# Optimization experiments

Hardware: AMD Instinct MI355X
Metric: run time of the kernel (lower is better)

## Reference

```python
import jax, jax.numpy as jnp
import numpy as np

B, H, W = 2, 192, 192
DIM, HEADS, WS = 192, 6, 16
NT, RD, GS = 128, 20, 128
MLP_HID, TD_F, KS = 384, 48, 5
EPS = 1e-5


def _layernorm(x, g, b):
    m = jnp.mean(x, -1, keepdims=True)
    v = jnp.var(x, -1, keepdims=True)
    return (x - m) / jnp.sqrt(v + EPS) * g + b


def _l2n(x):
    return x / jnp.maximum(jnp.linalg.norm(x, axis=-1, keepdims=True), 1e-12)


def _rpi(ws):
    coords = np.stack(np.meshgrid(np.arange(ws), np.arange(ws), indexing='ij'))
    cf = coords.reshape(2, -1)
    rc = (cf[:, :, None] - cf[:, None, :]).transpose(1, 2, 0)
    rc[..., 0] += ws - 1
    rc[..., 1] += ws - 1
    rc[..., 0] *= 2 * ws - 1
    return rc.sum(-1)  # (ws*ws, ws*ws)


RPI = _rpi(WS)


def _win_attn(qkv, rpb, proj_w, h, w):
    # plain W-MSA (shift_size = 0 -> no mask, no roll)
    b, n, c3 = qkv.shape
    c = c3 // 3
    hd = c // HEADS
    nw = WS * WS
    xw = qkv.reshape(b, h // WS, WS, w // WS, WS, c3).transpose(0, 1, 3, 2, 4, 5).reshape(-1, nw, c3)
    bw = xw.shape[0]
    q, k, v = xw.reshape(bw, nw, 3, HEADS, hd).transpose(2, 0, 3, 1, 4)
    attn = (q * hd ** -0.5) @ k.swapaxes(-2, -1)  # (bw, heads, nw, nw)
    bias = rpb[RPI.reshape(-1)].reshape(nw, nw, HEADS).transpose(2, 0, 1)
    attn = jax.nn.softmax(attn + bias[None])
    out = (attn @ v).swapaxes(1, 2).reshape(bw, nw, c) @ proj_w
    out = out.reshape(b, h // WS, w // WS, WS, WS, c).transpose(0, 1, 3, 2, 4, 5).reshape(b, n, c)
    return out


def _atd_ca(x, td, wq, wk, wv, scale_p):
    q = _l2n(x @ wq)   # (b,n,rd)
    k = _l2n(td @ wk)  # (b,m,rd)
    v = td @ wv        # (b,m,c)
    scale = 1.0 + jnp.clip(scale_p, 0.0, 3.0) * np.log(NT)
    attn = jax.nn.softmax((q @ k.swapaxes(-2, -1)) * scale)  # (b,n,m)
    return attn @ v, attn


def _ac_msa(qkv, tk_id, proj_w):
    b, n, c3 = qkv.shape
    c = c3 // 3
    gs = min(n, GS)
    ng = (n + gs - 1) // gs
    pad = ng * gs - n
    idx = jnp.argsort(tk_id, axis=-1)          # sort tokens by category id
    inv = jnp.argsort(idx, axis=-1)            # inverse permutation
    sq = jnp.take_along_axis(qkv, idx[..., None], axis=1)
    if pad > 0:
        sq = jnp.concatenate([sq, sq[:, n - pad:n][:, ::-1]], axis=1)
    q, k, v = sq.reshape(b, ng, gs, 3, HEADS, c // HEADS).transpose(3, 0, 1, 4, 2, 5)
    attn = jax.nn.softmax((q @ k.swapaxes(-2, -1)) * (c // HEADS) ** -0.5)
    out = (attn @ v).transpose(0, 1, 3, 2, 4).reshape(b, ng * gs, c)[:, :n]
    out = jnp.take_along_axis(out, inv[..., None], axis=1)
    return out @ proj_w


def _convffn(x, x_td, w1, dw, w2, h, w):
    y = jnp.concatenate([jax.nn.gelu(x @ w1, approximate=False), x_td], axis=-1)
    b, n, ch = y.shape
    img = y.swapaxes(1, 2).reshape(b, ch, h, w)
    p = (KS - 1) // 2
    conv = jax.lax.conv_general_dilated(img, dw, (1, 1), [(p, p), (p, p)],
                                        dimension_numbers=('NCHW', 'OIHW', 'NCHW'),
                                        feature_group_count=ch)
    conv = jax.nn.gelu(conv, approximate=False).reshape(b, ch, n).swapaxes(1, 2)
    return (y + conv) @ w2


def setup_inputs():
    key = jax.random.key(0)
    ks = jax.random.split(key, 16)
    p = lambda k, s: jax.random.normal(k, s, jnp.float32) * 0.02
    return {
        'x': jax.random.normal(ks[0], (B, H * W, DIM), jnp.float32),
        'td': jax.random.normal(ks[1], (B, NT, DIM), jnp.float32),
        'norm1_g': jnp.ones((DIM,), jnp.float32), 'norm1_b': jnp.zeros((DIM,), jnp.float32),
        'norm2_g': jnp.ones((DIM,), jnp.float32), 'norm2_b': jnp.zeros((DIM,), jnp.float32),
        'wqkv': p(ks[2], (DIM, 3 * DIM)),
        'rpb': p(ks[3], ((2 * WS - 1) ** 2, HEADS)),
        'win_proj': p(ks[4], (DIM, DIM)),
        'atd_wq': p(ks[5], (DIM, RD)),
        'atd_wk': p(ks[6], (DIM, RD)),
        'atd_wv': p(ks[7], (DIM, DIM)),
        'atd_scale': jnp.ones((1,), jnp.float32),
        'aca_proj': p(ks[8], (DIM, DIM)),
        'fc_td_w': p(ks[9], (DIM, TD_F)),
        'ffn_w1': p(ks[10], (DIM, MLP_HID)),
        'ffn_dw': p(ks[11], (MLP_HID + TD_F, 1, KS, KS)),
        'ffn_w2': p(ks[12], (MLP_HID + TD_F, DIM)),
        'h': H, 'w': W,
    }


def reference(x, td, norm1_g, norm1_b, norm2_g, norm2_b, wqkv, rpb, win_proj,
              atd_wq, atd_wk, atd_wv, atd_scale, aca_proj, fc_td_w,
              ffn_w1, ffn_dw, ffn_w2, h, w):
    shortcut = x
    xn = _layernorm(x, norm1_g, norm1_b)
    qkv = xn @ wqkv  # (b, n, 3c)
    x_atd, sim = _atd_ca(xn, td, atd_wq, atd_wk, atd_wv, atd_scale)
    x_aca = _ac_msa(qkv, jnp.argmax(sim, axis=-1), aca_proj)
    x_win = _win_attn(qkv, rpb, win_proj, h, w)
    x = shortcut + x_win + x_atd + x_aca
    x_td = sim @ (td @ fc_td_w)  # (b, n, td_f): dictionary features routed by cross-attn weights
    x = x + _convffn(_layernorm(x, norm2_g, norm2_b), x_td, ffn_w1, ffn_dw, ffn_w2, h, w)
    return x
```

## Files before the change

kernel.cpp:

```cpp
#include <hip/hip_runtime.h>
#include <hip/hip_bf16.h>
#include <math.h>

#define NTOK 36864
#define NTOT 73728
#define CDIM 192
#define C3   576
#define NH   6
#define HD   32
#define RD   20
#define NTD  128
#define GSZ  128
#define NGRP 288
#define MLP  384
#define TDF  48
#define CH   432
#define RAWLD 384

typedef __hip_bfloat16 bf16;
typedef __attribute__((ext_vector_type(8))) short short8;
typedef __attribute__((ext_vector_type(4))) float f32x4;

__device__ __forceinline__ float gelu_f(float x) {
    return 0.5f * x * (1.0f + erff(x * 0.7071067811865475f));
}

__device__ __forceinline__ unsigned short f32_to_bf16u(float f) {
    unsigned int u = __float_as_uint(f);
    u = (u + 0x7FFFu + ((u >> 16) & 1u)) >> 16;
    return (unsigned short)u;
}

__device__ __forceinline__ unsigned pack2bf(float a, float b) {
    return (unsigned)f32_to_bf16u(a) | ((unsigned)f32_to_bf16u(b) << 16);
}

__device__ __forceinline__ float bfbits2f(unsigned short u) {
    return __uint_as_float(((unsigned)u) << 16);
}

__global__ void pack_bt(const float* __restrict__ src, bf16* __restrict__ dst,
                        int K, int N, int ldk, int koff) {
    int i = blockIdx.x * 256 + threadIdx.x;
    if (i >= K * N) return;
    int k = i / N, n = i - k * N;
    dst[(long)n * ldk + koff + k] = __float2bfloat16(src[i]);
}

template<int WF32>
__global__ void ln_kernel(const float* __restrict__ x, const float* __restrict__ g,
                          const float* __restrict__ be, float* __restrict__ outf,
                          bf16* __restrict__ outh) {
    long tok = (long)blockIdx.x * 4 + (threadIdx.x >> 6);
    int lane = threadIdx.x & 63;
    const float* row = x + tok * CDIM;
    float v0 = row[lane], v1 = row[lane + 64], v2 = row[lane + 128];
    float s  = v0 + v1 + v2;
    float ss = v0 * v0 + v1 * v1 + v2 * v2;
    #pragma unroll
    for (int o = 32; o > 0; o >>= 1) {
        s  += __shfl_down(s, o);
        ss += __shfl_down(ss, o);
    }
    s = __shfl(s, 0); ss = __shfl(ss, 0);
    float mean = s * (1.0f / 192.0f);
    float var  = ss * (1.0f / 192.0f) - mean * mean;
    float rstd = rsqrtf(var + 1e-5f);
    float r0 = (v0 - mean) * rstd * g[lane]       + be[lane];
    float r1 = (v1 - mean) * rstd * g[lane + 64]  + be[lane + 64];
    float r2 = (v2 - mean) * rstd * g[lane + 128] + be[lane + 128];
    if (WF32) {
        float* orow = outf + tok * CDIM;
        orow[lane] = r0; orow[lane + 64] = r1; orow[lane + 128] = r2;
    }
    bf16* hrow = outh + tok * CDIM;
    hrow[lane]       = __float2bfloat16(r0);
    hrow[lane + 64]  = __float2bfloat16(r1);
    hrow[lane + 128] = __float2bfloat16(r2);
}

#define LDT 72
template<int ACC, int GELU, int BF16OUT, int CHUNK8, int ADDX, int PL8OUT = 0>
__global__ void __launch_bounds__(256) gemm_bt(
        const bf16* __restrict__ A, const bf16* __restrict__ Bt,
        void* __restrict__ Cv, const float* __restrict__ Xadd,
        int M, int N, int K, int lda, int ldbt, int ldc) {
    __shared__ short As[128 * LDT];
    __shared__ short Bs[64 * LDT];
    int tid  = threadIdx.x;
    int lane = tid & 63;
    int w    = tid >> 6;
    int wr = w >> 1, wc = w & 1;
    int row0 = blockIdx.y * 128, col0 = blockIdx.x * 64;
    int fr = lane & 15, fq = lane >> 4;
    f32x4 acc[4][2];
    #pragma unroll
    for (int m = 0; m < 4; ++m)
        #pragma unroll
        for (int n = 0; n < 2; ++n) acc[m][n] = (f32x4)(0.0f);

    int sa_row = tid >> 3;
    int sa_kc  = (tid & 7) * 8;
    int sb_col = tid & 63;
    int sb_kb  = (tid >> 6) * 16;
    bool cok = (col0 + sb_col) < N;

    for (int k0 = 0; k0 < K; k0 += 64) {
        __syncthreads();
        int kk = k0 + sa_kc;
        #pragma unroll
        for (int p = 0; p < 4; ++p) {
            int r = sa_row + p * 32;
            short8 v = (short8)(0);
            if (kk + 8 <= K) {
                const bf16* src;
                if (CHUNK8)
                    src = A + ((long)(kk >> 3) * NTOT + row0 + r) * 8;
                else
                    src = A + (long)(row0 + r) * lda + kk;
                v = *(const short8*)src;
            } else if (!CHUNK8 && kk < K) {
                #pragma unroll
                for (int i = 0; i < 8; ++i)
                    v[i] = (kk + i < K) ? *(const short*)&A[(long)(row0 + r) * lda + kk + i]
                                        : (short)0;
            }
            *(short8*)&As[r * LDT + sa_kc] = v;
        }
        {
            short8 v0 = (short8)(0), v1 = (short8)(0);
            if (cok) {
                const bf16* src = Bt + (long)(col0 + sb_col) * ldbt + k0 + sb_kb;
                v0 = *(const short8*)src;
                v1 = *(const short8*)(src + 8);
            }
            *(short8*)&Bs[sb_col * LDT + sb_kb]     = v0;
            *(short8*)&Bs[sb_col * LDT + sb_kb + 8] = v1;
        }
        __syncthreads();
        short8 af[4][2], bf_[2][2];
        #pragma unroll
        for (int m = 0; m < 4; ++m) {
            int r = wr * 64 + m * 16 + fr;
            af[m][0] = *(const short8*)&As[r * LDT + fq * 8];
            af[m][1] = *(const short8*)&As[r * LDT + 32 + fq * 8];
        }
        #pragma unroll
        for (int n = 0; n < 2; ++n) {
            int c = wc * 32 + n * 16 + fr;
            bf_[n][0] = *(const short8*)&Bs[c * LDT + fq * 8];
            bf_[n][1] = *(const short8*)&Bs[c * LDT + 32 + fq * 8];
        }
        #pragma unroll
        for (int m = 0; m < 4; ++m)
            #pragma unroll
            for (int n = 0; n < 2; ++n) {
                acc[m][n] = __builtin_amdgcn_mfma_f32_16x16x32_bf16(
                                af[m][0], bf_[n][0], acc[m][n], 0, 0, 0);
                acc[m][n] = __builtin_amdgcn_mfma_f32_16x16x32_bf16(
                                af[m][1], bf_[n][1], acc[m][n], 0, 0, 0);
            }
    }
    #pragma unroll
    for (int m = 0; m < 4; ++m) {
        #pragma unroll
        for (int n = 0; n < 2; ++n) {
            int gc = col0 + wc * 32 + n * 16 + fr;
            if (gc >= N) continue;
            #pragma unroll
            for (int r = 0; r < 4; ++r) {
                int gr = row0 + wr * 64 + m * 16 + fq * 4 + r;
                float vv = acc[m][n][r];
                if (GELU) vv = gelu_f(vv);
                if (BF16OUT) {
                    long o;
                    if (PL8OUT) o = ((long)(gc >> 3) * NTOT + gr) * 8 + (gc & 7);
                    else        o = (long)gr * ldc + gc;
                    ((bf16*)Cv)[o] = __float2bfloat16(vv);
                } else {
                    long o = (long)gr * ldc + gc;
                    float* Cc = (float*)Cv;
                    if (ADDX) Cc[o] = Xadd[o] + vv;
                    else if (ACC) Cc[o] += vv;
                    else Cc[o] = vv;
                }
            }
        }
    }
}

template<int ACC, int GELU>
__global__ void __launch_bounds__(256) gemm_kernel(
        const float* __restrict__ A, const float* __restrict__ B,
        float* __restrict__ Cc, int M, int N, int K, int lda, int ldb, int ldc) {
    __shared__ float As[16][68];
    __shared__ float Bs[16][68];
    int tid = threadIdx.x;
    int tr = tid >> 4, tc = tid & 15;
    int row0 = blockIdx.y * 64, col0 = blockIdx.x * 64;
    float acc[4][4] = {};
    int lm = tid >> 4;
    int lk = tid & 15;
    int bk = tid >> 6;
    int bn = tid & 63;
    for (int k0 = 0; k0 < K; k0 += 16) {
        #pragma unroll
        for (int i = 0; i < 4; ++i) {
            int m = lm + i * 16;
            int gr = row0 + m;
            As[lk][m] = (gr < M) ? A[(long)gr * lda + (k0 + lk)] : 0.0f;
        }
        #pragma unroll
        for (int i = 0; i < 4; ++i) {
            int kk = bk + i * 4;
            int gc = col0 + bn;
            Bs[kk][bn] = (gc < N) ? B[(long)(k0 + kk) * ldb + gc] : 0.0f;
        }
        __syncthreads();
        #pragma unroll
        for (int kk = 0; kk < 16; ++kk) {
            float4 av = *(const float4*)&As[kk][tr * 4];
            float4 bv = *(const float4*)&Bs[kk][tc * 4];
            float a[4] = {av.x, av.y, av.z, av.w};
            float b[4] = {bv.x, bv.y, bv.z, bv.w};
            #pragma unroll
            for (int i = 0; i < 4; ++i)
                #pragma unroll
                for (int j = 0; j < 4; ++j)
                    acc[i][j] = fmaf(a[i], b[j], acc[i][j]);
        }
        __syncthreads();
    }
    #pragma unroll
    for (int i = 0; i < 4; ++i) {
        int gr = row0 + tr * 4 + i;
        if (gr >= M) continue;
        #pragma unroll
        for (int j = 0; j < 4; ++j) {
            int gc = col0 + tc * 4 + j;
            if (gc >= N) continue;
            float v = acc[i][j];
            if (GELU) v = gelu_f(v);
            long o = (long)gr * ldc + gc;
            if (ACC) Cc[o] += v; else Cc[o] = v;
        }
    }
}

__global__ void __launch_bounds__(256) qn_kernel(
        const float* __restrict__ xn, const float* __restrict__ awq,
        float* __restrict__ qn) {
    __shared__ float aw[192 * RD];
    __shared__ float xs[256 * 33];
    int tid = threadIdx.x;
    long tok0 = (long)blockIdx.x * 256;
    for (int e = tid; e < 192 * RD; e += 256) aw[e] = awq[e];
    float acc[RD];
    #pragma unroll
    for (int j = 0; j < RD; ++j) acc[j] = 0.0f;
    for (int kc = 0; kc < 192; kc += 32) {
        __syncthreads();
        for (int e = tid; e < 256 * 32; e += 256) {
            int tk = e >> 5, kk = e & 31;
            xs[tk * 33 + kk] = xn[(tok0 + tk) * CDIM + kc + kk];
        }
        __syncthreads();
        #pragma unroll 8
        for (int kk = 0; kk < 32; ++kk) {
            float v = xs[tid * 33 + kk];
            const float* ar = &aw[(kc + kk) * RD];
            #pragma unroll
            for (int j = 0; j < RD; ++j) acc[j] = fmaf(v, ar[j], acc[j]);
        }
    }
    float ss = 0.0f;
    #pragma unroll
    for (int j = 0; j < RD; ++j) ss += acc[j] * acc[j];
    float inv = 1.0f / fmaxf(sqrtf(ss), 1e-12f);
    float* orow = qn + (tok0 + tid) * RD;
    #pragma unroll
    for (int j = 0; j < RD; ++j) orow[j] = acc[j] * inv;
}

__global__ void l2n_kernel(float* __restrict__ d, int nrows) {
    int i = blockIdx.x * blockDim.x + threadIdx.x;
    if (i >= nrows) return;
    float* r = d + (long)i * RD;
    float ss = 0.0f;
    #pragma unroll
    for (int k = 0; k < RD; ++k) ss += r[k] * r[k];
    float inv = 1.0f / fmaxf(sqrtf(ss), 1e-12f);
    #pragma unroll
    for (int k = 0; k < RD; ++k) r[k] *= inv;
}

__global__ void __launch_bounds__(128) sim_kernel(
        const float* __restrict__ qn, const float* __restrict__ kn,
        const float* __restrict__ scale_p, bf16* __restrict__ sim,
        int* __restrict__ tkid) {
    int tok = blockIdx.x;
    int b = tok / NTOK;
    int j = threadIdx.x;
    __shared__ float qv[RD];
    __shared__ float wred[4];
    __shared__ int   wredi[2];
    if (j < RD) qv[j] = qn[(long)tok * RD + j];
    __syncthreads();
    const float* kr = kn + ((long)b * NTD + j) * RD;
    float s = 0.0f;
    #pragma unroll
    for (int r = 0; r < RD; ++r) s = fmaf(qv[r], kr[r], s);
    float scl = 1.0f + fminf(fmaxf(scale_p[0], 0.0f), 3.0f) * logf(128.0f);
    s *= scl;
    float m = s; int mi = j;
    #pragma unroll
    for (int o = 32; o > 0; o >>= 1) {
        float om = __shfl_down(m, o); int oi = __shfl_down(mi, o);
        if (om > m || (om == m && oi < mi)) { m = om; mi = oi; }
    }
    int wv = j >> 6;
    if ((j & 63) == 0) { wred[wv] = m; wredi[wv] = mi; }
    __syncthreads();
    float m0 = wred[0], m1 = wred[1];
    float gm; int gi;
    if (m1 > m0) { gm = m1; gi = wredi[1]; } else { gm = m0; gi = wredi[0]; }
    float p = __expf(s - gm);
    float t = p;
    #pragma unroll
    for (int o = 32; o > 0; o >>= 1) t += __shfl_down(t, o);
    if ((j & 63) == 0) wred[2 + wv] = t;
    __syncthreads();
    float tot = wred[2] + wred[3];
    sim[(long)tok * NTD + j] = __float2bfloat16(p / tot);
    if (j == 0) tkid[tok] = gi;
}

__global__ void hist_kernel(const int* __restrict__ tkid, int* __restrict__ hist) {
    int tile = blockIdx.x;
    int tid = threadIdx.x;
    __shared__ int h[NTD];
    h[tid] = 0;
    __syncthreads();
    atomicAdd(&h[tkid[tile * GSZ + tid]], 1);
    __syncthreads();
    hist[tile * NTD + tid] = h[tid];
}

__global__ void scan_kernel(int* __restrict__ hist) {
    int b = blockIdx.x;
    int c = threadIdx.x;
    __shared__ int tot[NTD];
    __shared__ int base[NTD];
    int run = 0;
    for (int t = 0; t < NGRP; ++t) {
        int id = (b * NGRP + t) * NTD + c;
        int v = hist[id];
        hist[id] = run;
        run += v;
    }
    tot[c] = run;
    __syncthreads();
    if (c == 0) {
        int a = 0;
        for (int i = 0; i < NTD; ++i) { base[i] = a; a += tot[i]; }
    }
    __syncthreads();
    int bc = base[c];
    for (int t = 0; t < NGRP; ++t)
        hist[(b * NGRP + t) * NTD + c] += bc;
}

__global__ void scatter_kernel(const int* __restrict__ tkid, const int* __restrict__ hist,
                               int* __restrict__ idxs) {
    int tile = blockIdx.x;
    int b = tile / NGRP;
    int gl = tile % NGRP;
    int tid = threadIdx.x;
    __shared__ int cats[GSZ];
    int cat = tkid[tile * GSZ + tid];
    cats[tid] = cat;
    __syncthreads();
    int rank = 0;
    for (int j = 0; j < tid; ++j) rank += (cats[j] == cat) ? 1 : 0;
    int pos = hist[tile * NTD + cat] + rank;
    idxs[b * NTOK + pos] = gl * GSZ + tid;
}

#define VLDW 264
#define VLDA 136


__global__ void __launch_bounds__(256) win_mfma(
        const bf16* __restrict__ qkv, const float* __restrict__ rpb,
        bf16* __restrict__ raw) {
    int t2  = blockIdx.x;
    int h   = t2 % NH;
    int wid = t2 / NH;
    int b = wid / 144;
    int wrem = wid % 144;
    int wy = wrem / 12, wx = wrem % 12;
    long base_tok = (long)b * NTOK;

    __shared__ short Kt[256 * 40];
    __shared__ short Vt[32 * VLDW];
    __shared__ float rb[961];

    int tid = threadIdx.x;
    int lane = tid & 63;
    int wv = tid >> 6;
    int fr = lane & 15, fq = lane >> 4;
    const float scl = 0.17677669529663687f;

    for (int i = tid; i < 961; i += 256) rb[i] = rpb[i * NH + h];

    short8 qf[4];
    #pragma unroll
    for (int m = 0; m < 4; ++m) {
        int q = wv * 64 + m * 16 + fr;
        long nq = base_tok + (long)(wy * 16 + (q >> 4)) * 192 + (wx * 16 + (q & 15));
        qf[m] = *(const short8*)(qkv + nq * C3 + h * HD + fq * 8);
    }

    {
        int s_ = tid >> 2, ch = tid & 3;
        #pragma unroll
        for (int t = 0; t < 4; ++t) {
            int p = t * 64 + s_;
            long nk = base_tok + (long)(wy * 16 + (p >> 4)) * 192 + (wx * 16 + (p & 15));
            const bf16* kb = qkv + nk * C3 + CDIM + h * HD + ch * 8;
            *(short8*)&Kt[p * 40 + ch * 8] = *(const short8*)kb;
            short8 vv = *(const short8*)(kb + CDIM);
            #pragma unroll
            for (int i = 0; i < 8; ++i)
                Vt[(ch * 8 + i) * VLDW + p] = vv[i];
        }
    }
    __syncthreads();

    f32x4 acc[4][2];
    float lst[4];
    #pragma unroll
    for (int m = 0; m < 4; ++m) {
        acc[m][0] = (f32x4)(0.0f); acc[m][1] = (f32x4)(0.0f);
        lst[m] = 0.0f;
    }

    for (int t = 0; t < 4; ++t) {
        short8 ak[4], av[2][2];
        #pragma unroll
        for (int c = 0; c < 4; ++c)
            ak[c] = *(const short8*)&Kt[(t * 64 + c * 16 + fr) * 40 + fq * 8];
        #pragma unroll
        for (int n = 0; n < 2; ++n)
            #pragma unroll
            for (int ks = 0; ks < 2; ++ks)
                av[n][ks] = *(const short8*)&Vt[(n * 16 + fr) * VLDW + t * 64 + ks * 32 + fq * 8];

        #pragma unroll
        for (int m = 0; m < 4; ++m) {
            int q = wv * 64 + m * 16 + fr;
            int iy = q >> 4, ix = q & 15;
            int bxb = ix + 15 - 4 * fq;
            float s[4][4];
            #pragma unroll
            for (int c = 0; c < 4; ++c) {
                f32x4 s4 = (f32x4)(0.0f);
                s4 = __builtin_amdgcn_mfma_f32_16x16x32_bf16(ak[c], qf[m], s4, 0, 0, 0);
                const float* rbp = &rb[(iy + 15 - (t * 4 + c)) * 31 + bxb];
                #pragma unroll
                for (int r = 0; r < 4; ++r)
                    s[c][r] = s4[r] * scl + rbp[-r];
            }
            float ps = 0.0f;
            #pragma unroll
            for (int c = 0; c < 4; ++c)
                #pragma unroll
                for (int r = 0; r < 4; ++r) {
                    float p = __expf(s[c][r]);
                    s[c][r] = p;
                    ps += p;
                }
            ps += __shfl_xor(ps, 16);
            ps += __shfl_xor(ps, 32);
            lst[m] += ps;
            unsigned pk[4][2];
            #pragma unroll
            for (int c = 0; c < 4; ++c) {
                pk[c][0] = pack2bf(s[c][0], s[c][1]);
                pk[c][1] = pack2bf(s[c][2], s[c][3]);
            }
            #pragma unroll
            for (int ks = 0; ks < 2; ++ks) {
                unsigned u[4];
                #pragma unroll
                for (int jj = 0; jj < 4; ++jj) {
                    int src = fr + 16 * (2 * (fq & 1) + (jj >> 1));
                    unsigned lo = (unsigned)__shfl((int)pk[2 * ks][jj & 1], src);
                    unsigned hi = (unsigned)__shfl((int)pk[2 * ks + 1][jj & 1], src);
                    u[jj] = (fq & 2) ? hi : lo;
                }
                short8 pb;
                #pragma unroll
                for (int jj = 0; jj < 4; ++jj) {
                    pb[2 * jj]     = (short)(u[jj] & 0xFFFF);
                    pb[2 * jj + 1] = (short)(u[jj] >> 16);
                }
                #pragma unroll
                for (int n = 0; n < 2; ++n)
                    acc[m][n] = __builtin_amdgcn_mfma_f32_16x16x32_bf16(
                                    av[n][ks], pb, acc[m][n], 0, 0, 0);
            }
        }
    }
    #pragma unroll
    for (int m = 0; m < 4; ++m) {
        int q = wv * 64 + m * 16 + fr;
        long nq = base_tok + (long)(wy * 16 + (q >> 4)) * 192 + (wx * 16 + (q & 15));
        float inv = 1.0f / lst[m];
        #pragma unroll
        for (int n = 0; n < 2; ++n) {
            uint2 wv2;
            wv2.x = pack2bf(acc[m][n][0] * inv, acc[m][n][1] * inv);
            wv2.y = pack2bf(acc[m][n][2] * inv, acc[m][n][3] * inv);
            *(uint2*)(raw + nq * RAWLD + h * HD + n * 16 + 4 * fq) = wv2;
        }
    }
}

__global__ void __launch_bounds__(128) aca_mfma(
        const bf16* __restrict__ qkv, const int* __restrict__ idxs,
        bf16* __restrict__ raw) {
    int t2   = blockIdx.x;
    int h    = t2 % NH;
    int grp  = t2 / NH;
    int b = grp / NGRP;
    int g = grp % NGRP;
    long btok = (long)b * NTOK;

    __shared__ short Kt[128 * 40];
    __shared__ short Vt[32 * VLDA];
    __shared__ int   sidx[GSZ];

    int tid = threadIdx.x;
    int lane = tid & 63;
    int half = tid >> 6;
    int fr = lane & 15, fq = lane >> 4;
    const float scl = 0.17677669529663687f;

    sidx[tid] = idxs[btok + g * GSZ + tid];
    __syncthreads();

    short8 qf[4];
    #pragma unroll
    for (int m = 0; m < 4; ++m) {
        long n = btok + sidx[half * 64 + m * 16 + fr];
        qf[m] = *(const short8*)(qkv + n * C3 + h * HD + fq * 8);
    }

    {
        int s_ = tid >> 1, hf = tid & 1;
        int d0 = hf * 16;
        #pragma unroll
        for (int t = 0; t < 2; ++t) {
            int p = t * 64 + s_;
            long n = btok + sidx[p];
            const bf16* kb = qkv + n * C3 + CDIM + h * HD + d0;
            *(short8*)&Kt[p * 40 + d0]     = *(const short8*)kb;
            *(short8*)&Kt[p * 40 + d0 + 8] = *(const short8*)(kb + 8);
            short8 v0 = *(const short8*)(kb + CDIM);
            short8 v1 = *(const short8*)(kb + CDIM + 8);
            #pragma unroll
            for (int i = 0; i < 8; ++i) {
                Vt[(d0 + i) * VLDA + p]     = v0[i];
                Vt[(d0 + 8 + i) * VLDA + p] = v1[i];
            }
        }
    }
    __syncthreads();

    f32x4 acc[4][2];
    float lst[4];
    #pragma unroll
    for (int m = 0; m < 4; ++m) {
        acc[m][0] = (f32x4)(0.0f); acc[m][1] = (f32x4)(0.0f);
        lst[m] = 0.0f;
    }

    for (int t = 0; t < 2; ++t) {
        short8 ak[4], av[2][2];
        #pragma unroll
        for (int c = 0; c < 4; ++c)
            ak[c] = *(const short8*)&Kt[(t * 64 + c * 16 + fr) * 40 + fq * 8];
        #pragma unroll
        for (int n = 0; n < 2; ++n)
            #pragma unroll
            for (int ks = 0; ks < 2; ++ks)
                av[n][ks] = *(const short8*)&Vt[(n * 16 + fr) * VLDA + t * 64 + ks * 32 + fq * 8];

        #pragma unroll
        for (int m = 0; m < 4; ++m) {
            float s[4][4];
            #pragma unroll
            for (int c = 0; c < 4; ++c) {
                f32x4 s4 = (f32x4)(0.0f);
                s4 = __builtin_amdgcn_mfma_f32_16x16x32_bf16(ak[c], qf[m], s4, 0, 0, 0);
                #pragma unroll
                for (int r = 0; r < 4; ++r) s[c][r] = s4[r] * scl;
            }
            float ps = 0.0f;
            #pragma unroll
            for (int c = 0; c < 4; ++c)
                #pragma unroll
                for (int r = 0; r < 4; ++r) {
                    float p = __expf(s[c][r]);
                    s[c][r] = p;
                    ps += p;
                }
            ps += __shfl_xor(ps, 16);
            ps += __shfl_xor(ps, 32);
            lst[m] += ps;
            unsigned pk[4][2];
            #pragma unroll
            for (int c = 0; c < 4; ++c) {
                pk[c][0] = pack2bf(s[c][0], s[c][1]);
                pk[c][1] = pack2bf(s[c][2], s[c][3]);
            }
            #pragma unroll
            for (int ks = 0; ks < 2; ++ks) {
                unsigned u[4];
                #pragma unroll
                for (int jj = 0; jj < 4; ++jj) {
                    int src = fr + 16 * (2 * (fq & 1) + (jj >> 1));
                    unsigned lo = (unsigned)__shfl((int)pk[2 * ks][jj & 1], src);
                    unsigned hi = (unsigned)__shfl((int)pk[2 * ks + 1][jj & 1], src);
                    u[jj] = (fq & 2) ? hi : lo;
                }
                short8 pb;
                #pragma unroll
                for (int jj = 0; jj < 4; ++jj) {
                    pb[2 * jj]     = (short)(u[jj] & 0xFFFF);
                    pb[2 * jj + 1] = (short)(u[jj] >> 16);
                }
                #pragma unroll
                for (int n = 0; n < 2; ++n)
                    acc[m][n] = __builtin_amdgcn_mfma_f32_16x16x32_bf16(
                                    av[n][ks], pb, acc[m][n], 0, 0, 0);
            }
        }
    }
    #pragma unroll
    for (int m = 0; m < 4; ++m) {
        long n = btok + sidx[half * 64 + m * 16 + fr];
        float inv = 1.0f / lst[m];
        #pragma unroll
        for (int nn = 0; nn < 2; ++nn) {
            uint2 wv2;
            wv2.x = pack2bf(acc[m][nn][0] * inv, acc[m][nn][1] * inv);
            wv2.y = pack2bf(acc[m][nn][2] * inv, acc[m][nn][3] * inv);
            *(uint2*)(raw + n * RAWLD + CDIM + h * HD + nn * 16 + 4 * fq) = wv2;
        }
    }
}

__global__ void xtdcopy_kernel(const bf16* __restrict__ xtd, bf16* __restrict__ y) {
    long tok = (long)blockIdx.x * 256 + threadIdx.x;
    const uint4* src = (const uint4*)(xtd + tok * TDF);
    #pragma unroll
    for (int j = 0; j < 6; ++j)
        *(uint4*)(y + ((long)(48 + j) * NTOT + tok) * 8) = src[j];
}

#define CPS 1296
__global__ void __launch_bounds__(256) conv_kernel(
        const bf16* __restrict__ y, const float* __restrict__ dw,
        bf16* __restrict__ zc) {
    int bid = blockIdx.x;
    int ck   = bid % 54;
    int tile = (bid / 54) % 36;
    int b    = bid / (54 * 36);
    int ty = tile / 6, tx = tile % 6;
    int c0 = ck * 8;
    __shared__ float ys[8 * CPS];
    __shared__ float wt[8 * 25];
    int tid = threadIdx.x;
    const bf16* ypl = y + ((long)ck * NTOT + (long)b * NTOK) * 8;
    for (int p = tid; p < 1296; p += 256) {
        int ly = p / 36, lx = p - ly * 36;
        int gy = ty * 32 + ly - 2, gx = tx * 32 + lx - 2;
        float f[8];
        if (gy >= 0 && gy < 192 && gx >= 0 && gx < 192) {
            short8 hv = *(const short8*)(ypl + (long)(gy * 192 + gx) * 8);
            #pragma unroll
            for (int i = 0; i < 8; ++i) f[i] = bfbits2f((unsigned short)hv[i]);
        } else {
            #pragma unroll
            for (int i = 0; i < 8; ++i) f[i] = 0.0f;
        }
        #pragma unroll
        for (int i = 0; i < 8; ++i) ys[i * CPS + p] = f[i];
    }
    for (int e = tid; e < 200; e += 256) wt[e] = dw[c0 * 25 + e];
    __syncthreads();
    int col = tid & 31, r4 = tid >> 5;
    int py0 = r4 * 4;
    long tok0 = (long)b * NTOK + (long)(ty * 32 + py0) * 192 + tx * 32 + col;
    unsigned hh[4][4];
    for (int c = 0; c < 8; ++c) {
        const float* yc = &ys[c * CPS];
        float w[25];
        #pragma unroll
        for (int t = 0; t < 25; ++t) w[t] = wt[c * 25 + t];
        float a[4] = {0.0f, 0.0f, 0.0f, 0.0f};
        #pragma unroll
        for (int dy2 = 0; dy2 < 8; ++dy2) {
            float rv[5];
            #pragma unroll
            for (int dx = 0; dx < 5; ++dx)
                rv[dx] = yc[(py0 + dy2) * 36 + col + dx];
            #pragma unroll
            for (int i = 0; i < 4; ++i) {
                int dy = dy2 - i;
                if (dy >= 0 && dy < 5) {
                    #pragma unroll
                    for (int dx = 0; dx < 5; ++dx)
                        a[i] = fmaf(rv[dx], w[dy * 5 + dx], a[i]);
                }
            }
        }
        #pragma unroll
        for (int i = 0; i < 4; ++i) {
            float center = yc[(py0 + i + 2) * 36 + col + 2];
            unsigned short hsh = f32_to_bf16u(center + gelu_f(a[i]));
            if (c & 1) hh[i][c >> 1] |= ((unsigned)hsh) << 16;
            else       hh[i][c >> 1] = (unsigned)hsh;
        }
    }
    #pragma unroll
    for (int i = 0; i < 4; ++i) {
        long tok = tok0 + (long)i * 192;
        *(uint4*)(zc + ((long)ck * NTOT + tok) * 8) =
            make_uint4(hh[i][0], hh[i][1], hh[i][2], hh[i][3]);
    }
}

extern "C" void kernel_launch(void* const* d_in, const int* in_sizes, int n_in,
                              void* d_out, int out_size, void* d_ws, size_t ws_size,
                              hipStream_t stream) {
    (void)in_sizes; (void)n_in; (void)out_size; (void)ws_size;
    const float* x     = (const float*)d_in[0];
    const float* td    = (const float*)d_in[1];
    const float* n1g   = (const float*)d_in[2];
    const float* n1b   = (const float*)d_in[3];
    const float* n2g   = (const float*)d_in[4];
    const float* n2b   = (const float*)d_in[5];
    const float* wqkv  = (const float*)d_in[6];
    const float* rpb   = (const float*)d_in[7];
    const float* wproj = (const float*)d_in[8];
    const float* awq   = (const float*)d_in[9];
    const float* awk   = (const float*)d_in[10];
    const float* awv   = (const float*)d_in[11];
    const float* ascl  = (const float*)d_in[12];
    const float* aproj = (const float*)d_in[13];
    const float* fcw   = (const float*)d_in[14];
    const float* w1    = (const float*)d_in[15];
    const float* dw    = (const float*)d_in[16];
    const float* w2    = (const float*)d_in[17];
    float* out = (float*)d_out;

    char* ws = (char*)d_ws;
    size_t off = 0;
    auto alloc = [&](size_t bytes) -> char* {
        char* p = ws + off;
        off += (bytes + 255) & ~(size_t)255;
        return p;
    };
    bf16*  qkv  = (bf16*)alloc((size_t)NTOT * C3 * 2);
    float* xn   = (float*)alloc((size_t)NTOT * CDIM * 4);
    bf16*  xnh  = (bf16*)alloc((size_t)NTOT * CDIM * 2);
    float* qn   = (float*)alloc((size_t)NTOT * RD * 4);
    bf16*  simb = (bf16*)alloc((size_t)NTOT * NTD * 2);
    bf16*  xtd  = (bf16*)alloc((size_t)NTOT * TDF * 2);
    float* kn   = (float*)alloc((size_t)2 * NTD * RD * 4);
    float* vtd  = (float*)alloc((size_t)2 * NTD * CDIM * 4);
    float* tdf  = (float*)alloc((size_t)2 * NTD * TDF * 4);
    bf16*  vtdT = (bf16*)alloc((size_t)2 * CDIM * NTD * 2);
    bf16*  tdfT = (bf16*)alloc((size_t)2 * TDF * NTD * 2);
    bf16*  wqkvT= (bf16*)alloc((size_t)C3 * CDIM * 2);
    bf16*  projT= (bf16*)alloc((size_t)CDIM * 384 * 2);
    bf16*  w1T  = (bf16*)alloc((size_t)MLP * CDIM * 2);
    bf16*  w2T  = (bf16*)alloc((size_t)CDIM * 448 * 2);
    int*   tkid = (int*)alloc((size_t)NTOT * 4);
    int*   idxs = (int*)alloc((size_t)NTOT * 4);
    int*   hist = (int*)alloc((size_t)576 * NTD * 4);
    bf16*  y    = qkv;
    bf16*  raw  = (bf16*)xn;
    bf16*  zc   = (bf16*)xn;

    pack_bt<<<(192 * 576 + 255) / 256, 256, 0, stream>>>(wqkv, wqkvT, 192, 576, 192, 0);
    pack_bt<<<(192 * 192 + 255) / 256, 256, 0, stream>>>(wproj, projT, 192, 192, 384, 0);
    pack_bt<<<(192 * 192 + 255) / 256, 256, 0, stream>>>(aproj, projT, 192, 192, 384, 192);
    pack_bt<<<(192 * 384 + 255) / 256, 256, 0, stream>>>(w1, w1T, 192, 384, 192, 0);
    hipMemsetAsync(w2T, 0, (size_t)CDIM * 448 * 2, stream);
    pack_bt<<<(432 * 192 + 255) / 256, 256, 0, stream>>>(w2, w2T, 432, 192, 448, 0);

    ln_kernel<1><<<NTOT / 4, 256, 0, stream>>>(x, n1g, n1b, xn, xnh);

    gemm_bt<0,0,1,0,0><<<dim3(9, 576), 256, 0, stream>>>(
        xnh, wqkvT, qkv, nullptr, NTOT, C3, CDIM, CDIM, CDIM, C3);

    qn_kernel<<<NTOT / 256, 256, 0, stream>>>(xn, awq, qn);

    gemm_kernel<0,0><<<dim3(1, 4), 256, 0, stream>>>(td, awk, kn, 2 * NTD, RD, CDIM, CDIM, RD, RD);
    gemm_kernel<0,0><<<dim3(3, 4), 256, 0, stream>>>(td, awv, vtd, 2 * NTD, CDIM, CDIM, CDIM, CDIM, CDIM);
    gemm_kernel<0,0><<<dim3(1, 4), 256, 0, stream>>>(td, fcw, tdf, 2 * NTD, TDF, CDIM, CDIM, TDF, TDF);
    l2n_kernel<<<1, 256, 0, stream>>>(kn, 2 * NTD);
    for (int b = 0; b < 2; ++b) {
        pack_bt<<<(NTD * CDIM + 255) / 256, 256, 0, stream>>>(
            vtd + (size_t)b * NTD * CDIM, vtdT + (size_t)b * CDIM * NTD, NTD, CDIM, NTD, 0);
        pack_bt<<<(NTD * TDF + 255) / 256, 256, 0, stream>>>(
            tdf + (size_t)b * NTD * TDF, tdfT + (size_t)b * TDF * NTD, NTD, TDF, NTD, 0);
    }

    sim_kernel<<<NTOT, 128, 0, stream>>>(qn, kn, ascl, simb, tkid);

    for (int b = 0; b < 2; ++b) {
        gemm_bt<0,0,0,0,1><<<dim3(3, 288), 256, 0, stream>>>(
            simb + (size_t)b * NTOK * NTD, vtdT + (size_t)b * CDIM * NTD,
            out + (size_t)b * NTOK * CDIM, x + (size_t)b * NTOK * CDIM,
            NTOK, CDIM, NTD, NTD, NTD, CDIM);
        gemm_bt<0,0,1,0,0><<<dim3(1, 288), 256, 0, stream>>>(
            simb + (size_t)b * NTOK * NTD, tdfT + (size_t)b * TDF * NTD,
            xtd + (size_t)b * NTOK * TDF, nullptr, NTOK, TDF, NTD, NTD, NTD, TDF);
    }

    hist_kernel<<<576, 128, 0, stream>>>(tkid, hist);
    scan_kernel<<<2, 128, 0, stream>>>(hist);
    scatter_kernel<<<576, 128, 0, stream>>>(tkid, hist, idxs);

    win_mfma<<<288 * NH, 256, 0, stream>>>(qkv, rpb, raw);
    aca_mfma<<<576 * NH, 128, 0, stream>>>(qkv, idxs, raw);
    gemm_bt<1,0,0,0,0><<<dim3(3, 576), 256, 0, stream>>>(
        raw, projT, out, nullptr, NTOT, CDIM, 384, RAWLD, 384, CDIM);

    ln_kernel<0><<<NTOT / 4, 256, 0, stream>>>(out, n2g, n2b, nullptr, xnh);

    gemm_bt<0,1,1,0,0,1><<<dim3(6, 576), 256, 0, stream>>>(
        xnh, w1T, y, nullptr, NTOT, MLP, CDIM, CDIM, CDIM, 0);
    xtdcopy_kernel<<<NTOT / 256, 256, 0, stream>>>(xtd, y);

    conv_kernel<<<2 * 36 * 54, 256, 0, stream>>>(y, dw, zc);
    gemm_bt<1,0,0,1,0><<<dim3(3, 576), 256, 0, stream>>>(
        zc, w2T, out, nullptr, NTOT, CDIM, CH, 0, 448, CDIM);
}
```

Measured before the change: 778.7 us.

## Enlarge GEMM tile to 256x64 and use sigmoid-based GELU approximation

The bf16 MFMA GEMM now computes 256x64 tiles, with each wave owning 64 rows across all 64 columns, so B fragments are reused across four M sub-tiles and grids are halved. GELU switches from erf to a tanh-style sigmoid approximation with __expf. This is meant to raise arithmetic intensity per LDS load and cut epilogue cost. In exchange it adds more LDS and registers per block, lowers occupancy, leaves fewer blocks for small GEMMs, and introduces small numeric differences in GELU.

Measured after the change: 837.3 us. +7.5%, slower.

```diff
diff --git a/kernel.cpp b/kernel.cpp
--- a/kernel.cpp
+++ b/kernel.cpp
@@ -22,7 +22,8 @@
 typedef __attribute__((ext_vector_type(4))) float f32x4;
 
 __device__ __forceinline__ float gelu_f(float x) {
-    return 0.5f * x * (1.0f + erff(x * 0.7071067811865475f));
+    float u = x * (1.5957691216f + 0.0713548162f * x * x);
+    return x / (1.0f + __expf(-u));
 }
 
 __device__ __forceinline__ unsigned short f32_to_bf16u(float f) {
@@ -85,19 +86,18 @@
         const bf16* __restrict__ A, const bf16* __restrict__ Bt,
         void* __restrict__ Cv, const float* __restrict__ Xadd,
         int M, int N, int K, int lda, int ldbt, int ldc) {
-    __shared__ short As[128 * LDT];
+    __shared__ short As[256 * LDT];
     __shared__ short Bs[64 * LDT];
     int tid  = threadIdx.x;
     int lane = tid & 63;
     int w    = tid >> 6;
-    int wr = w >> 1, wc = w & 1;
-    int row0 = blockIdx.y * 128, col0 = blockIdx.x * 64;
+    int row0 = blockIdx.y * 256, col0 = blockIdx.x * 64;
     int fr = lane & 15, fq = lane >> 4;
-    f32x4 acc[4][2];
+    f32x4 acc[4][4];
     #pragma unroll
     for (int m = 0; m < 4; ++m)
         #pragma unroll
-        for (int n = 0; n < 2; ++n) acc[m][n] = (f32x4)(0.0f);
+        for (int n = 0; n < 4; ++n) acc[m][n] = (f32x4)(0.0f);
 
     int sa_row = tid >> 3;
     int sa_kc  = (tid & 7) * 8;
@@ -109,7 +109,7 @@
         __syncthreads();
         int kk = k0 + sa_kc;
         #pragma unroll
-        for (int p = 0; p < 4; ++p) {
+        for (int p = 0; p < 8; ++p) {
             int r = sa_row + p * 32;
             short8 v = (short8)(0);
             if (kk + 8 <= K) {
@@ -138,38 +138,32 @@
             *(short8*)&Bs[sb_col * LDT + sb_kb + 8] = v1;
         }
         __syncthreads();
-        short8 af[4][2], bf_[2][2];
-        #pragma unroll
-        for (int m = 0; m < 4; ++m) {
-            int r = wr * 64 + m * 16 + fr;
-            af[m][0] = *(const short8*)&As[r * LDT + fq * 8];
-            af[m][1] = *(const short8*)&As[r * LDT + 32 + fq * 8];
-        }
-        #pragma unroll
-        for (int n = 0; n < 2; ++n) {
-            int c = wc * 32 + n * 16 + fr;
-            bf_[n][0] = *(const short8*)&Bs[c * LDT + fq * 8];
-            bf_[n][1] = *(const short8*)&Bs[c * LDT + 32 + fq * 8];
-        }
-        #pragma unroll
-        for (int m = 0; m < 4; ++m)
-            #pragma unroll
-            for (int n = 0; n < 2; ++n) {
-                acc[m][n] = __builtin_amdgcn_mfma_f32_16x16x32_bf16(
-                                af[m][0], bf_[n][0], acc[m][n], 0, 0, 0);
-                acc[m][n] = __builtin_amdgcn_mfma_f32_16x16x32_bf16(
-                                af[m][1], bf_[n][1], acc[m][n], 0, 0, 0);
-            }
+        #pragma unroll
+        for (int kh = 0; kh < 2; ++kh) {
+            short8 af[4], bf_[4];
+            #pragma unroll
+            for (int m = 0; m < 4; ++m)
+                af[m] = *(const short8*)&As[(w * 64 + m * 16 + fr) * LDT + kh * 32 + fq * 8];
+            #pragma unroll
+            for (int n = 0; n < 4; ++n)
+                bf_[n] = *(const short8*)&Bs[(n * 16 + fr) * LDT + kh * 32 + fq * 8];
+            #pragma unroll
+            for (int m = 0; m < 4; ++m)
+                #pragma unroll
+                for (int n = 0; n < 4; ++n)
+                    acc[m][n] = __builtin_amdgcn_mfma_f32_16x16x32_bf16(
+                                    af[m], bf_[n], acc[m][n], 0, 0, 0);
+        }
     }
     #pragma unroll
     for (int m = 0; m < 4; ++m) {
         #pragma unroll
-        for (int n = 0; n < 2; ++n) {
-            int gc = col0 + wc * 32 + n * 16 + fr;
+        for (int n = 0; n < 4; ++n) {
+            int gc = col0 + n * 16 + fr;
             if (gc >= N) continue;
             #pragma unroll
             for (int r = 0; r < 4; ++r) {
-                int gr = row0 + wr * 64 + m * 16 + fq * 4 + r;
+                int gr = row0 + w * 64 + m * 16 + fq * 4 + r;
                 float vv = acc[m][n][r];
                 if (GELU) vv = gelu_f(vv);
                 if (BF16OUT) {
@@ -805,7 +799,7 @@
 
     ln_kernel<1><<<NTOT / 4, 256, 0, stream>>>(x, n1g, n1b, xn, xnh);
 
-    gemm_bt<0,0,1,0,0><<<dim3(9, 576), 256, 0, stream>>>(
+    gemm_bt<0,0,1,0,0><<<dim3(9, 288), 256, 0, stream>>>(
         xnh, wqkvT, qkv, nullptr, NTOT, C3, CDIM, CDIM, CDIM, C3);
 
     qn_kernel<<<NTOT / 256, 256, 0, stream>>>(xn, awq, qn);
@@ -824,11 +818,11 @@
     sim_kernel<<<NTOT, 128, 0, stream>>>(qn, kn, ascl, simb, tkid);
 
     for (int b = 0; b < 2; ++b) {
-        gemm_bt<0,0,0,0,1><<<dim3(3, 288), 256, 0, stream>>>(
+        gemm_bt<0,0,0,0,1><<<dim3(3, 144), 256, 0, stream>>>(
             simb + (size_t)b * NTOK * NTD, vtdT + (size_t)b * CDIM * NTD,
             out + (size_t)b * NTOK * CDIM, x + (size_t)b * NTOK * CDIM,
             NTOK, CDIM, NTD, NTD, NTD, CDIM);
-        gemm_bt<0,0,1,0,0><<<dim3(1, 288), 256, 0, stream>>>(
+        gemm_bt<0,0,1,0,0><<<dim3(1, 144), 256, 0, stream>>>(
             simb + (size_t)b * NTOK * NTD, tdfT + (size_t)b * TDF * NTD,
             xtd + (size_t)b * NTOK * TDF, nullptr, NTOK, TDF, NTD, NTD, NTD, TDF);
     }
@@ -839,16 +833,16 @@
 
     win_mfma<<<288 * NH, 256, 0, stream>>>(qkv, rpb, raw);
     aca_mfma<<<576 * NH, 128, 0, stream>>>(qkv, idxs, raw);
-    gemm_bt<1,0,0,0,0><<<dim3(3, 576), 256, 0, stream>>>(
+    gemm_bt<1,0,0,0,0><<<dim3(3, 288), 256, 0, stream>>>(
         raw, projT, out, nullptr, NTOT, CDIM, 384, RAWLD, 384, CDIM);
 
     ln_kernel<0><<<NTOT / 4, 256, 0, stream>>>(out, n2g, n2b, nullptr, xnh);
 
-    gemm_bt<0,1,1,0,0,1><<<dim3(6, 576), 256, 0, stream>>>(
+    gemm_bt<0,1,1,0,0,1><<<dim3(6, 288), 256, 0, stream>>>(
         xnh, w1T, y, nullptr, NTOT, MLP, CDIM, CDIM, CDIM, 0);
     xtdcopy_kernel<<<NTOT / 256, 256, 0, stream>>>(xtd, y);
 
     conv_kernel<<<2 * 36 * 54, 256, 0, stream>>>(y, dw, zc);
-    gemm_bt<1,0,0,1,0><<<dim3(3, 576), 256, 0, stream>>>(
+    gemm_bt<1,0,0,1,0><<<dim3(3, 288), 256, 0, stream>>>(
         zc, w2T, out, nullptr, NTOT, CDIM, CH, 0, 448, CDIM);
 }
```
